# Optimization experiments

Measured on AMD Instinct MI355X. Metric: run time of the kernel, lower is better.

## Reference

```python
import jax, jax.numpy as jnp
import numpy as np

ENC_DIM, DEC_DIM, HID_DIM = 512, 1024, 128
B, T = 64, 2048


def setup_inputs() -> dict:
    key = jax.random.key(0)
    ks = jax.random.split(key, 8)
    encoder_outs = jax.random.normal(ks[0], (B, T, ENC_DIM), dtype=jnp.float32)
    decoder_state = jax.random.normal(ks[1], (B, DEC_DIM), dtype=jnp.float32)
    mask = jax.random.randint(ks[2], (B, T), 0, 2) == 1
    # parameters (torch nn.Linear: y = x @ W.T + b)
    sV = 1.0 / np.sqrt(ENC_DIM)
    sW = 1.0 / np.sqrt(DEC_DIM)
    sw = 1.0 / np.sqrt(HID_DIM)
    V_w = jax.random.uniform(ks[3], (HID_DIM, ENC_DIM), minval=-sV, maxval=sV)
    V_b = jax.random.uniform(ks[4], (HID_DIM,), minval=-sV, maxval=sV)
    W_w = jax.random.uniform(ks[5], (HID_DIM, DEC_DIM), minval=-sW, maxval=sW)
    w_w = jax.random.uniform(ks[6], (1, HID_DIM), minval=-sw, maxval=sw)
    w_b = jax.random.uniform(ks[7], (1,), minval=-sw, maxval=sw)
    return {"encoder_outs": encoder_outs, "decoder_state": decoder_state,
            "mask": mask, "V_w": V_w, "V_b": V_b, "W_w": W_w,
            "w_w": w_w, "w_b": w_b}


def reference(encoder_outs, decoder_state, mask, V_w, V_b, W_w, w_w, w_b):
    # [B,1,H] query projection + [B,T,H] key projection
    q = jnp.einsum('bd,hd->bh', decoder_state, W_w)[:, None, :]
    k = jnp.einsum('bte,he->bth', encoder_outs, V_w) + V_b
    # scores: [B,T]
    erg = jnp.einsum('bth,h->bt', jnp.tanh(q + k), w_w[0]) + w_b[0]
    erg = jnp.where(mask, -jnp.inf, erg)
    attention_weights = jax.nn.softmax(erg, axis=1)
    attention_context = jnp.einsum('bte,bt->be', encoder_outs, attention_weights)
    return (attention_context, attention_weights)
```

## Files before the change

kernel.cpp:

```cpp
#include <hip/hip_runtime.h>
#include <hip/hip_bf16.h>

#define Bn   64
#define Tn   2048
#define ENCD 512
#define DECD 1024
#define HIDD 128
#define TT   32
#define NCH  (Tn / TT)
#define LROW 520

typedef __attribute__((ext_vector_type(8))) short bf16x8;
typedef __attribute__((ext_vector_type(4))) float f32x4;

__device__ __forceinline__ unsigned short f2bf(float f) {
    union { float f; unsigned u; } v; v.f = f;
    unsigned r = v.u + 0x7FFFu + ((v.u >> 16) & 1u);
    return (unsigned short)(r >> 16);
}
__device__ __forceinline__ float bf2f(unsigned short s) {
    union { unsigned u; float f; } v; v.u = ((unsigned)s) << 16;
    return v.f;
}
__device__ __forceinline__ float tanh_fast(float x) {
    float xa = fminf(fmaxf(x, -10.f), 10.f);
    float e = __expf(2.f * xa);
    return (e - 1.f) / (e + 1.f);
}

__global__ __launch_bounds__(256) void prep(
    const float* __restrict__ dec, const float* __restrict__ Ww,
    const float* __restrict__ Vb,  const float* __restrict__ Vw,
    float* __restrict__ qb, unsigned short* __restrict__ Vbf)
{
    const int blk = blockIdx.x, tid = threadIdx.x;
    if (blk < 512) {
        const int b = blk >> 3, hg = blk & 7;
        const int h_local = tid >> 4, seg = tid & 15;
        const int h = hg * 16 + h_local;
        const float4* w = (const float4*)(Ww + (size_t)h * DECD);
        const float4* d = (const float4*)(dec + (size_t)b * DECD);
        float acc = 0.f;
        #pragma unroll
        for (int j = 0; j < 16; ++j) {
            int f4 = j * 16 + seg;
            float4 a = d[f4], bb = w[f4];
            acc += a.x * bb.x + a.y * bb.y + a.z * bb.z + a.w * bb.w;
        }
        acc += __shfl_xor(acc, 1);
        acc += __shfl_xor(acc, 2);
        acc += __shfl_xor(acc, 4);
        acc += __shfl_xor(acc, 8);
        if (seg == 0) qb[b * HIDD + h] = acc + Vb[h];
    } else {
        const int c = blk - 512;
        const float4* src = (const float4*)Vw;
        #pragma unroll
        for (int i = 0; i < 2; ++i) {
            int f4 = c * 512 + tid * 2 + i;
            float4 v = src[f4];
            ushort4 u;
            u.x = f2bf(v.x); u.y = f2bf(v.y); u.z = f2bf(v.z); u.w = f2bf(v.w);
            *(ushort4*)&Vbf[f4 * 4] = u;
        }
    }
}

__global__ __launch_bounds__(512, 8) void attn_main(
    const float* __restrict__ enc, const int* __restrict__ mask,
    const float* __restrict__ qb,  const unsigned short* __restrict__ Vbf,
    const float* __restrict__ ww,  const float* __restrict__ wb,
    float* __restrict__ pW, float* __restrict__ mC, float* __restrict__ lC,
    float* __restrict__ ctxP)
{
    __shared__ unsigned short encS[TT * LROW];
    __shared__ float wpart[8][TT];
    __shared__ float pS[TT];

    const int chunk = blockIdx.x, b = blockIdx.y;
    const int tid = threadIdx.x;
    const int t0 = chunk * TT;
    const int wave = tid >> 6, lane = tid & 63;
    const int li = lane & 15, quad = lane >> 4;

    const int h = wave * 16 + li;
    const float qv = qb[b * HIDD + h];
    const float wv = ww[h];

    const float* encTile = enc + ((size_t)b * Tn + t0) * ENCD;
    {
        float4 v[8];
        #pragma unroll
        for (int it = 0; it < 8; ++it)
            v[it] = ((const float4*)encTile)[it * 512 + tid];
        #pragma unroll
        for (int it = 0; it < 8; ++it) {
            int f4 = it * 512 + tid;
            int t = f4 >> 7, e = (f4 & 127) * 4;
            ushort4 u;
            u.x = f2bf(v[it].x); u.y = f2bf(v[it].y);
            u.z = f2bf(v[it].z); u.w = f2bf(v[it].w);
            *(ushort4*)&encS[t * LROW + e] = u;
        }
    }
    __syncthreads();

    f32x4 acc[2];
    acc[0] = (f32x4){0.f, 0.f, 0.f, 0.f};
    acc[1] = (f32x4){0.f, 0.f, 0.f, 0.f};
    const unsigned short* vrow = Vbf + (size_t)h * ENCD;

    #pragma unroll 4
    for (int ks = 0; ks < 16; ++ks) {
        int k0 = ks * 32 + quad * 8;
        bf16x8 a0 = *(const bf16x8*)&encS[(0  + li) * LROW + k0];
        bf16x8 a1 = *(const bf16x8*)&encS[(16 + li) * LROW + k0];
        bf16x8 bb = *(const bf16x8*)(vrow + k0);
        acc[0] = __builtin_amdgcn_mfma_f32_16x16x32_bf16(a0, bb, acc[0], 0, 0, 0);
        acc[1] = __builtin_amdgcn_mfma_f32_16x16x32_bf16(a1, bb, acc[1], 0, 0, 0);
    }

    #pragma unroll
    for (int mt = 0; mt < 2; ++mt)
        #pragma unroll
        for (int r = 0; r < 4; ++r) {
            float s = tanh_fast(acc[mt][r] + qv) * wv;
            s += __shfl_xor(s, 1);
            s += __shfl_xor(s, 2);
            s += __shfl_xor(s, 4);
            s += __shfl_xor(s, 8);
            if (li == 0) wpart[wave][mt * 16 + quad * 4 + r] = s;
        }
    __syncthreads();

    if (wave == 0) {
        float e = -INFINITY;
        if (lane < TT) {
            int t = lane;
            float v = wb[0];
            #pragma unroll
            for (int w = 0; w < 8; ++w) v += wpart[w][t];
            e = (mask[b * Tn + t0 + t] != 0) ? -INFINITY : v;
        }
        float m = e;
        #pragma unroll
        for (int off = 32; off >= 1; off >>= 1)
            m = fmaxf(m, __shfl_xor(m, off));
        float p = (e == -INFINITY) ? 0.f : __expf(e - m);
        float l = p;
        #pragma unroll
        for (int off = 32; off >= 1; off >>= 1)
            l += __shfl_xor(l, off);
        if (lane < TT) {
            pS[lane] = p;
            pW[(size_t)b * Tn + t0 + lane] = p;
        }
        if (lane == 0) {
            mC[b * NCH + chunk] = m;
            lC[b * NCH + chunk] = l;
        }
    }
    __syncthreads();

    {
        float c = 0.f;
        #pragma unroll 8
        for (int t = 0; t < TT; ++t)
            c += pS[t] * bf2f(encS[t * LROW + tid]);
        ctxP[((size_t)(b * NCH + chunk)) * ENCD + tid] = c;
    }
}

__global__ __launch_bounds__(256) void finalize(
    const float* __restrict__ mC, const float* __restrict__ lC,
    const float* __restrict__ pW, const float* __restrict__ ctxP,
    float* __restrict__ out)
{
    __shared__ float scaleS[NCH];
    __shared__ float invLs;
    __shared__ float red[256];
    const int b = blockIdx.x, part = blockIdx.y, tid = threadIdx.x;
    const int wave = tid >> 6, lane = tid & 63;

    if (wave == 0) {
        float m = mC[b * NCH + lane];
        float l = lC[b * NCH + lane];
        float gm = m;
        #pragma unroll
        for (int off = 32; off >= 1; off >>= 1)
            gm = fmaxf(gm, __shfl_xor(gm, off));
        float sc = (m == -INFINITY) ? 0.f : __expf(m - gm);
        float ls = l * sc;
        #pragma unroll
        for (int off = 32; off >= 1; off >>= 1)
            ls += __shfl_xor(ls, off);
        scaleS[lane] = sc;
        if (lane == 0) invLs = 1.f / ls;
    }
    __syncthreads();
    const float invL = invLs;

    if (part < 4) {
        const int e = part * 128 + (tid & 127);
        const int half = tid >> 7;
        float c = 0.f;
        #pragma unroll 8
        for (int cc = half * 32; cc < half * 32 + 32; ++cc)
            c += scaleS[cc] * ctxP[((size_t)(b * NCH + cc)) * ENCD + e];
        red[tid] = c;
        __syncthreads();
        if (tid < 128) {
            int ee = part * 128 + tid;
            out[b * ENCD + ee] = (red[tid] + red[tid + 128]) * invL;
        }
    } else {
        float* outw = out + Bn * ENCD;
        #pragma unroll
        for (int i = 0; i < 8; ++i) {
            int t = i * 256 + tid;
            outw[(size_t)b * Tn + t] = pW[(size_t)b * Tn + t] * scaleS[t >> 5] * invL;
        }
    }
}

extern "C" void kernel_launch(void* const* d_in, const int* in_sizes, int n_in,
                              void* d_out, int out_size, void* d_ws, size_t ws_size,
                              hipStream_t stream)
{
    const float* enc  = (const float*)d_in[0];
    const float* dec  = (const float*)d_in[1];
    const int*   mask = (const int*)d_in[2];
    const float* Vw   = (const float*)d_in[3];
    const float* Vb   = (const float*)d_in[4];
    const float* Ww   = (const float*)d_in[5];
    const float* ww   = (const float*)d_in[6];
    const float* wb   = (const float*)d_in[7];
    float* out = (float*)d_out;
    float* ws  = (float*)d_ws;

    float*          qb   = ws;
    unsigned short* Vbf  = (unsigned short*)(ws + 8192);
    float*          pW   = ws + 40960;
    float*          mC   = ws + 172032;
    float*          lC   = ws + 176128;
    float*          ctxP = ws + 180224;

    hipLaunchKernelGGL(prep, dim3(576), dim3(256), 0, stream, dec, Ww, Vb, Vw, qb, Vbf);
    hipLaunchKernelGGL(attn_main, dim3(NCH, Bn), dim3(512), 0, stream,
                       enc, mask, qb, Vbf, ww, wb, pW, mC, lC, ctxP);
    hipLaunchKernelGGL(finalize, dim3(Bn, 5), dim3(256), 0, stream, mC, lC, pW, ctxP, out);
}
```

Baseline: 390.8 us.

## Drop per-chunk max in softmax and broadcast probabilities via shuffles

Since the scores come from a tanh weighted by w_w, they are bounded, so the kernel computes exp(score) directly. This removes the per-chunk max, the mC buffer and the rescaling in finalize. Probabilities are passed to the context accumulation with __shfl instead of shared memory, which drops one __syncthreads. Encoder tile loads become nontemporal and are split into two batches, and ctxP is written with nontemporal stores. The risk is exp overflow when the weights w_w and w_b are large, which the old max-subtraction guarded against.

```diff
diff --git a/kernel.cpp b/kernel.cpp
--- a/kernel.cpp
+++ b/kernel.cpp
@@ -27,6 +27,9 @@
     float e = __expf(2.f * xa);
     return (e - 1.f) / (e + 1.f);
 }
+__device__ __forceinline__ f32x4 ldnt4(const float* p) {
+    return __builtin_nontemporal_load((const f32x4*)p);
+}
 
 __global__ __launch_bounds__(256) void prep(
     const float* __restrict__ dec, const float* __restrict__ Ww,
@@ -38,13 +41,14 @@
         const int b = blk >> 3, hg = blk & 7;
         const int h_local = tid >> 4, seg = tid & 15;
         const int h = hg * 16 + h_local;
-        const float4* w = (const float4*)(Ww + (size_t)h * DECD);
-        const float4* d = (const float4*)(dec + (size_t)b * DECD);
+        const float* w = Ww + (size_t)h * DECD;
+        const float* d = dec + (size_t)b * DECD;
         float acc = 0.f;
         #pragma unroll
         for (int j = 0; j < 16; ++j) {
             int f4 = j * 16 + seg;
-            float4 a = d[f4], bb = w[f4];
+            f32x4 a = *(const f32x4*)(d + f4 * 4);
+            f32x4 bb = *(const f32x4*)(w + f4 * 4);
             acc += a.x * bb.x + a.y * bb.y + a.z * bb.z + a.w * bb.w;
         }
         acc += __shfl_xor(acc, 1);
@@ -54,15 +58,11 @@
         if (seg == 0) qb[b * HIDD + h] = acc + Vb[h];
     } else {
         const int c = blk - 512;
-        const float4* src = (const float4*)Vw;
-        #pragma unroll
-        for (int i = 0; i < 2; ++i) {
-            int f4 = c * 512 + tid * 2 + i;
-            float4 v = src[f4];
-            ushort4 u;
-            u.x = f2bf(v.x); u.y = f2bf(v.y); u.z = f2bf(v.z); u.w = f2bf(v.w);
-            *(ushort4*)&Vbf[f4 * 4] = u;
-        }
+        int f4 = c * 256 + tid;
+        f32x4 v = *(const f32x4*)(Vw + f4 * 4);
+        ushort4 u;
+        u.x = f2bf(v.x); u.y = f2bf(v.y); u.z = f2bf(v.z); u.w = f2bf(v.w);
+        *(ushort4*)&Vbf[f4 * 4] = u;
     }
 }
 
@@ -70,12 +70,10 @@
     const float* __restrict__ enc, const int* __restrict__ mask,
     const float* __restrict__ qb,  const unsigned short* __restrict__ Vbf,
     const float* __restrict__ ww,  const float* __restrict__ wb,
-    float* __restrict__ pW, float* __restrict__ mC, float* __restrict__ lC,
-    float* __restrict__ ctxP)
+    float* __restrict__ pW, float* __restrict__ lC, float* __restrict__ ctxP)
 {
     __shared__ unsigned short encS[TT * LROW];
     __shared__ float wpart[8][TT];
-    __shared__ float pS[TT];
 
     const int chunk = blockIdx.x, b = blockIdx.y;
     const int tid = threadIdx.x;
@@ -86,20 +84,23 @@
     const int h = wave * 16 + li;
     const float qv = qb[b * HIDD + h];
     const float wv = ww[h];
-
-    const float* encTile = enc + ((size_t)b * Tn + t0) * ENCD;
-    {
-        float4 v[8];
-        #pragma unroll
-        for (int it = 0; it < 8; ++it)
-            v[it] = ((const float4*)encTile)[it * 512 + tid];
-        #pragma unroll
-        for (int it = 0; it < 8; ++it) {
-            int f4 = it * 512 + tid;
+    const float wbv = wb[0];
+    const int mk = (lane < TT) ? mask[b * Tn + t0 + lane] : 1;
+
+    const float* src = enc + ((size_t)b * Tn + t0) * ENCD;
+    #pragma unroll
+    for (int batch = 0; batch < 2; ++batch) {
+        f32x4 v[4];
+        #pragma unroll
+        for (int j = 0; j < 4; ++j)
+            v[j] = ldnt4(src + ((batch * 4 + j) * 512 + tid) * 4);
+        #pragma unroll
+        for (int j = 0; j < 4; ++j) {
+            int f4 = (batch * 4 + j) * 512 + tid;
             int t = f4 >> 7, e = (f4 & 127) * 4;
             ushort4 u;
-            u.x = f2bf(v[it].x); u.y = f2bf(v[it].y);
-            u.z = f2bf(v[it].z); u.w = f2bf(v[it].w);
+            u.x = f2bf(v[j].x); u.y = f2bf(v[j].y);
+            u.z = f2bf(v[j].z); u.w = f2bf(v[j].w);
             *(ushort4*)&encS[t * LROW + e] = u;
         }
     }
@@ -133,69 +134,49 @@
         }
     __syncthreads();
 
+    float p = 0.f;
+    if (lane < TT) {
+        float v = wbv;
+        #pragma unroll
+        for (int w = 0; w < 8; ++w) v += wpart[w][lane];
+        p = (mk != 0) ? 0.f : __expf(v);
+    }
+
     if (wave == 0) {
-        float e = -INFINITY;
-        if (lane < TT) {
-            int t = lane;
-            float v = wb[0];
-            #pragma unroll
-            for (int w = 0; w < 8; ++w) v += wpart[w][t];
-            e = (mask[b * Tn + t0 + t] != 0) ? -INFINITY : v;
-        }
-        float m = e;
-        #pragma unroll
-        for (int off = 32; off >= 1; off >>= 1)
-            m = fmaxf(m, __shfl_xor(m, off));
-        float p = (e == -INFINITY) ? 0.f : __expf(e - m);
         float l = p;
         #pragma unroll
         for (int off = 32; off >= 1; off >>= 1)
             l += __shfl_xor(l, off);
-        if (lane < TT) {
-            pS[lane] = p;
-            pW[(size_t)b * Tn + t0 + lane] = p;
-        }
-        if (lane == 0) {
-            mC[b * NCH + chunk] = m;
-            lC[b * NCH + chunk] = l;
-        }
-    }
-    __syncthreads();
+        if (lane < TT) pW[(size_t)b * Tn + t0 + lane] = p;
+        if (lane == 0) lC[b * NCH + chunk] = l;
+    }
 
     {
         float c = 0.f;
-        #pragma unroll 8
-        for (int t = 0; t < TT; ++t)
-            c += pS[t] * bf2f(encS[t * LROW + tid]);
-        ctxP[((size_t)(b * NCH + chunk)) * ENCD + tid] = c;
+        #pragma unroll
+        for (int t = 0; t < TT; ++t) {
+            float pt = __shfl(p, t);
+            c += pt * bf2f(encS[t * LROW + tid]);
+        }
+        __builtin_nontemporal_store(c, &ctxP[((size_t)(b * NCH + chunk)) * ENCD + tid]);
     }
 }
 
 __global__ __launch_bounds__(256) void finalize(
-    const float* __restrict__ mC, const float* __restrict__ lC,
-    const float* __restrict__ pW, const float* __restrict__ ctxP,
-    float* __restrict__ out)
-{
-    __shared__ float scaleS[NCH];
+    const float* __restrict__ lC, const float* __restrict__ pW,
+    const float* __restrict__ ctxP, float* __restrict__ out)
+{
     __shared__ float invLs;
     __shared__ float red[256];
     const int b = blockIdx.x, part = blockIdx.y, tid = threadIdx.x;
     const int wave = tid >> 6, lane = tid & 63;
 
     if (wave == 0) {
-        float m = mC[b * NCH + lane];
         float l = lC[b * NCH + lane];
-        float gm = m;
         #pragma unroll
         for (int off = 32; off >= 1; off >>= 1)
-            gm = fmaxf(gm, __shfl_xor(gm, off));
-        float sc = (m == -INFINITY) ? 0.f : __expf(m - gm);
-        float ls = l * sc;
-        #pragma unroll
-        for (int off = 32; off >= 1; off >>= 1)
-            ls += __shfl_xor(ls, off);
-        scaleS[lane] = sc;
-        if (lane == 0) invLs = 1.f / ls;
+            l += __shfl_xor(l, off);
+        if (lane == 0) invLs = 1.f / l;
     }
     __syncthreads();
     const float invL = invLs;
@@ -206,7 +187,7 @@
         float c = 0.f;
         #pragma unroll 8
         for (int cc = half * 32; cc < half * 32 + 32; ++cc)
-            c += scaleS[cc] * ctxP[((size_t)(b * NCH + cc)) * ENCD + e];
+            c += ctxP[((size_t)(b * NCH + cc)) * ENCD + e];
         red[tid] = c;
         __syncthreads();
         if (tid < 128) {
@@ -218,7 +199,7 @@
         #pragma unroll
         for (int i = 0; i < 8; ++i) {
             int t = i * 256 + tid;
-            outw[(size_t)b * Tn + t] = pW[(size_t)b * Tn + t] * scaleS[t >> 5] * invL;
+            outw[(size_t)b * Tn + t] = pW[(size_t)b * Tn + t] * invL;
         }
     }
 }
@@ -241,12 +222,11 @@
     float*          qb   = ws;
     unsigned short* Vbf  = (unsigned short*)(ws + 8192);
     float*          pW   = ws + 40960;
-    float*          mC   = ws + 172032;
-    float*          lC   = ws + 176128;
+    float*          lC   = ws + 172032;
     float*          ctxP = ws + 180224;
 
     hipLaunchKernelGGL(prep, dim3(576), dim3(256), 0, stream, dec, Ww, Vb, Vw, qb, Vbf);
     hipLaunchKernelGGL(attn_main, dim3(NCH, Bn), dim3(512), 0, stream,
-                       enc, mask, qb, Vbf, ww, wb, pW, mC, lC, ctxP);
-    hipLaunchKernelGGL(finalize, dim3(Bn, 5), dim3(256), 0, stream, mC, lC, pW, ctxP, out);
-}
+                       enc, mask, qb, Vbf, ww, wb, pW, lC, ctxP);
+    hipLaunchKernelGGL(finalize, dim3(Bn, 5), dim3(256), 0, stream, lC, pW, ctxP, out);
+}
```

Result: no change. 395.8 us (+1.3%).
